# Kernel tuning notes

Measured on AMD Instinct MI355X. Metric: run time of the kernel, lower is better.

## Reference

```python
import jax, jax.numpy as jnp
import numpy as np

# Criterion init constants
WEIGHT_START = 1e-3
WEIGHT_MAX = 5e3
START_RAMPUP = 50000
N_RAMPUP = 100000
EPS = 1e-3

B, N_CLOTH, M_OBS, N_FACES = 2, 16384, 12000, 16384


def setup_inputs() -> dict:
    key = jax.random.key(0)
    ks = jax.random.split(key, 5)
    return dict(
        cloth_curr_pos=jax.random.normal(ks[0], (B, N_CLOTH, 3), jnp.float32),
        cloth_next_pos=jax.random.normal(ks[1], (B, N_CLOTH, 3), jnp.float32),
        obstacle_curr_pos=jax.random.normal(ks[2], (B, M_OBS, 3), jnp.float32),
        obstacle_next_pos=jax.random.normal(ks[3], (B, M_OBS, 3), jnp.float32),
        obstacle_faces=jax.random.randint(ks[4], (B, N_FACES, 3), 0, M_OBS, dtype=jnp.int64),
        iter_num=60000,
    )


def _face_normals(verts, faces):
    # verts: [M,3], faces: [F,3] -> normalized face normals [F,3]
    v = verts[faces]  # [F,3(vert),3(xyz)]
    n = jnp.cross(v[:, 1] - v[:, 0], v[:, 2] - v[:, 0])
    return n / (jnp.linalg.norm(n, axis=-1, keepdims=True) + 1e-12)


def _calc_loss(curr_pos, next_pos, obs_curr, obs_next, faces):
    # face centroids at current obstacle positions: [F,3]
    face_curr = obs_curr[faces].mean(axis=-2)
    # brute-force KNN (K=1): squared euclidean distances [N,F]
    d2 = (
        jnp.sum(curr_pos * curr_pos, axis=-1, keepdims=True)
        - 2.0 * curr_pos @ face_curr.T
        + jnp.sum(face_curr * face_curr, axis=-1)[None, :]
    )
    nn_idx = jnp.argmin(d2, axis=-1)  # [N]
    # face centroids / normals at next obstacle positions
    face_next = obs_next[faces].mean(axis=-2)  # [F,3]
    fn = _face_normals(obs_next, faces)        # [F,3]
    nn_points = face_next[nn_idx]   # [N,3]
    nn_normals = fn[nn_idx]         # [N,3]
    distance = jnp.sum((next_pos - nn_points) * nn_normals, axis=-1)  # [N]
    interpenetration = jnp.maximum(EPS - distance, 0.0) ** 3
    return interpenetration.sum(), interpenetration


def reference(cloth_curr_pos, cloth_next_pos, obstacle_curr_pos, obstacle_next_pos, obstacle_faces, iter_num):
    # weight ramp (Python scalar math, matches get_weight)
    it = max(iter_num - START_RAMPUP, 0)
    progress = min(it / N_RAMPUP, 1.0)
    weight = WEIGHT_START + (WEIGHT_MAX - WEIGHT_START) * progress

    losses, per_verts = jax.vmap(_calc_loss)(
        cloth_curr_pos, cloth_next_pos, obstacle_curr_pos, obstacle_next_pos, obstacle_faces
    )
    b = cloth_curr_pos.shape[0]
    loss = losses.sum() / b * weight          # scalar
    per_vert = per_verts.sum(axis=0) / b * weight  # [N]
    return loss, per_vert
```

## Files before the change

kernel.cpp:

```cpp
#include <hip/hip_runtime.h>
#include <math.h>

#define B_ 2
#define N_ 16384
#define M_ 12000
#define F_ 16384

#define P_ 128
#define TILE_ 128

typedef short bf16x8 __attribute__((ext_vector_type(8)));
typedef float f32x16 __attribute__((ext_vector_type(16)));

__device__ __host__ inline unsigned short bf16rn(float x) {
  unsigned int u = __float_as_uint(x);
  u = (u + 0x7FFFu + ((u >> 16) & 1u)) >> 16;
  return (unsigned short)u;
}
__device__ inline float bf16tof(unsigned short h) {
  return __uint_as_float(((unsigned int)h) << 16);
}

__global__ __launch_bounds__(256) void face_precomp(
    const float* __restrict__ obs_curr,
    const float* __restrict__ obs_next,
    const int* __restrict__ faces,
    float4* __restrict__ fcurr,
    float4* __restrict__ fnext,
    uint4* __restrict__ fpack,
    float* __restrict__ out) {
  int t = blockIdx.x * 256 + threadIdx.x;
  if (t == 0) out[0] = 0.0f;
  if (t >= B_ * F_) return;
  int b = t / F_;
  const float* oc = obs_curr + (size_t)b * M_ * 3;
  const float* on = obs_next + (size_t)b * M_ * 3;
  int i0 = faces[3 * (size_t)t + 0];
  int i1 = faces[3 * (size_t)t + 1];
  int i2 = faces[3 * (size_t)t + 2];

  float ax = oc[3*i0], ay = oc[3*i0+1], az = oc[3*i0+2];
  float bx = oc[3*i1], by = oc[3*i1+1], bz = oc[3*i1+2];
  float cx = oc[3*i2], cy = oc[3*i2+1], cz = oc[3*i2+2];
  float gx = (ax + bx + cx) / 3.0f;
  float gy = (ay + by + cy) / 3.0f;
  float gz = (az + bz + cz) / 3.0f;
  float w = gx*gx + gy*gy + gz*gz;
  fcurr[t] = make_float4(gx, gy, gz, w);

  float fx = -2.0f * gx, fy = -2.0f * gy, fz = -2.0f * gz;
  unsigned short fhx = bf16rn(fx), flx = bf16rn(fx - bf16tof(fhx));
  unsigned short fhy = bf16rn(fy), fly = bf16rn(fy - bf16tof(fhy));
  unsigned short fhz = bf16rn(fz), flz = bf16rn(fz - bf16tof(fhz));
  unsigned short whi = bf16rn(w),  wlo = bf16rn(w - bf16tof(whi));
  uint4 r0, r1;
  r0.x = (unsigned)fhx | ((unsigned)flx << 16);
  r0.y = r0.x;
  r0.z = (unsigned)fhy | ((unsigned)fly << 16);
  r0.w = r0.z;
  r1.x = (unsigned)fhz | ((unsigned)flz << 16);
  r1.y = r1.x;
  r1.z = (unsigned)whi | ((unsigned)wlo << 16);
  r1.w = 0;
  fpack[(size_t)t * 2 + 0] = r0;
  fpack[(size_t)t * 2 + 1] = r1;

  float nax = on[3*i0], nay = on[3*i0+1], naz = on[3*i0+2];
  float nbx = on[3*i1], nby = on[3*i1+1], nbz = on[3*i1+2];
  float ncx = on[3*i2], ncy = on[3*i2+1], ncz = on[3*i2+2];
  float hx = (nax + nbx + ncx) / 3.0f;
  float hy = (nay + nby + ncy) / 3.0f;
  float hz = (naz + nbz + ncz) / 3.0f;
  float e1x = nbx - nax, e1y = nby - nay, e1z = nbz - naz;
  float e2x = ncx - nax, e2y = ncy - nay, e2z = ncz - naz;
  float crx = e1y * e2z - e1z * e2y;
  float cry = e1z * e2x - e1x * e2z;
  float crz = e1x * e2y - e1y * e2x;
  float len = sqrtf(crx*crx + cry*cry + crz*crz);
  float inv = 1.0f / (len + 1e-12f);
  fnext[2 * (size_t)t + 0] = make_float4(hx, hy, hz, 0.0f);
  fnext[2 * (size_t)t + 1] = make_float4(crx*inv, cry*inv, crz*inv, 0.0f);
}

__global__ __launch_bounds__(256, 4) void knn_mfma32(
    const float* __restrict__ cloth_curr,
    const uint4* __restrict__ fpack,
    float* __restrict__ pmin) {
  int bid = blockIdx.x;
  int s   = bid & 7;
  int vgb = (bid >> 3) & 127;
  int b   = bid >> 10;
  int lane = threadIdx.x & 63;
  int wid  = threadIdx.x >> 6;
  int h = lane >> 5;
  int m = lane & 31;
  int vw = vgb * 128 + wid * 32;

  const float* cp = cloth_curr + ((size_t)b * N_ + vw + m) * 3;
  float cxx = cp[0], cyy = cp[1], czz = cp[2];
  unsigned short chx = bf16rn(cxx), clx = bf16rn(cxx - bf16tof(chx));
  unsigned short chy = bf16rn(cyy), cly = bf16rn(cyy - bf16tof(chy));
  unsigned short chz = bf16rn(czz), clz = bf16rn(czz - bf16tof(chz));
  const short one = (short)0x3F80;
  bf16x8 bfrag;
  if (h == 0) {
    bfrag[0] = (short)chx; bfrag[1] = (short)chx;
    bfrag[2] = (short)clx; bfrag[3] = (short)clx;
    bfrag[4] = (short)chy; bfrag[5] = (short)chy;
    bfrag[6] = (short)cly; bfrag[7] = (short)cly;
  } else {
    bfrag[0] = (short)chz; bfrag[1] = (short)chz;
    bfrag[2] = (short)clz; bfrag[3] = (short)clz;
    bfrag[4] = one; bfrag[5] = one;
    bfrag[6] = 0;   bfrag[7] = 0;
  }

  f32x16 zc;
#pragma unroll
  for (int k = 0; k < 16; ++k) zc[k] = 0.0f;

  const uint4* fp = fpack + ((size_t)b * F_ + (size_t)s * 2048 + m) * 2 + h;
  float* pout = pmin + ((size_t)(b * P_ + s * 16)) * N_ + vw + m;

  for (int part = 0; part < 16; ++part) {
    uint4 a0 = fp[0];
    uint4 a1 = fp[64];
    uint4 a2 = fp[128];
    uint4 a3 = fp[192];
    fp += 256;
    f32x16 d0 = __builtin_amdgcn_mfma_f32_32x32x16_bf16(
        __builtin_bit_cast(bf16x8, a0), bfrag, zc, 0, 0, 0);
    f32x16 d1 = __builtin_amdgcn_mfma_f32_32x32x16_bf16(
        __builtin_bit_cast(bf16x8, a1), bfrag, zc, 0, 0, 0);
    f32x16 d2 = __builtin_amdgcn_mfma_f32_32x32x16_bf16(
        __builtin_bit_cast(bf16x8, a2), bfrag, zc, 0, 0, 0);
    f32x16 d3 = __builtin_amdgcn_mfma_f32_32x32x16_bf16(
        __builtin_bit_cast(bf16x8, a3), bfrag, zc, 0, 0, 0);

    float r[8];
#pragma unroll
    for (int k = 0; k < 8; ++k) {
      float v = fminf(fminf(d0[k], d0[k + 8]), d1[k]);
      v = fminf(fminf(v, d1[k + 8]), d2[k]);
      v = fminf(fminf(v, d2[k + 8]), d3[k]);
      v = fminf(v, d3[k + 8]);
      r[k] = v;
    }
    float t1 = fminf(fminf(r[0], r[1]), r[2]);
    t1 = fminf(fminf(t1, r[3]), r[4]);
    t1 = fminf(fminf(t1, r[5]), r[6]);
    float bmin = fminf(t1, r[7]);
    bmin = fminf(bmin, __shfl_xor(bmin, 32, 64));
    if (lane < 32) *pout = bmin;
    pout += N_;
  }
}

__global__ __launch_bounds__(256) void epilogue(
    const float* __restrict__ cloth_curr,
    const float* __restrict__ cloth_next,
    const float4* __restrict__ fcurr,
    const float4* __restrict__ fnext,
    const float* __restrict__ pmin,
    const int* __restrict__ iter_num,
    float* __restrict__ out) {
  int t = blockIdx.x * 256 + threadIdx.x;
  int i = t >> 1;
  int b = t & 1;

  int it = *iter_num;
  double itc = (double)(it - 50000);
  if (itc < 0.0) itc = 0.0;
  double prog = itc / 100000.0;
  if (prog > 1.0) prog = 1.0;
  float weight = (float)(1e-3 + (5e3 - 1e-3) * prog);
  float scale = weight * 0.5f;

  float best = 3.4e38f;
  int bp = 0;
#pragma unroll 8
  for (int p = 0; p < P_; ++p) {
    float s = pmin[((size_t)(b * P_ + p)) * N_ + i];
    bool mm = s < best;
    best = mm ? s : best;
    bp = mm ? p : bp;
  }

  const float* cp = cloth_curr + ((size_t)b * N_ + i) * 3;
  float m2x = -2.0f * cp[0];
  float m2y = -2.0f * cp[1];
  float m2z = -2.0f * cp[2];
  const float4* fpp = fcurr + (size_t)b * F_ + (size_t)bp * TILE_;
  float sbest = 3.4e38f;
  int jwin = 0;
#pragma unroll 4
  for (int j = 0; j < TILE_; ++j) {
    float4 fc = fpp[j];
    float s = fmaf(m2x, fc.x, fmaf(m2y, fc.y, fmaf(m2z, fc.z, fc.w)));
    bool u = s < sbest;
    sbest = u ? s : sbest;
    jwin = u ? j : jwin;
  }
  int fidx = bp * TILE_ + jwin;

  float4 cent = fnext[2 * ((size_t)b * F_ + fidx) + 0];
  float4 nrm  = fnext[2 * ((size_t)b * F_ + fidx) + 1];
  const float* np2 = cloth_next + ((size_t)b * N_ + i) * 3;
  float dist = (np2[0] - cent.x) * nrm.x +
               (np2[1] - cent.y) * nrm.y +
               (np2[2] - cent.z) * nrm.z;
  float ip = fmaxf(1e-3f - dist, 0.0f);
  float acc = ip * ip * ip * scale;

  float pair = acc + __shfl_xor(acc, 1, 64);
  if (b == 0) out[1 + i] = pair;

  float r = acc;
#pragma unroll
  for (int off = 32; off > 0; off >>= 1) r += __shfl_down(r, off, 64);
  __shared__ float wsum[4];
  int lane = threadIdx.x & 63;
  int w = threadIdx.x >> 6;
  if (lane == 0) wsum[w] = r;
  __syncthreads();
  if (threadIdx.x == 0)
    atomicAdd(out, (wsum[0] + wsum[1]) + (wsum[2] + wsum[3]));
}

extern "C" void kernel_launch(void* const* d_in, const int* in_sizes, int n_in,
                              void* d_out, int out_size, void* d_ws, size_t ws_size,
                              hipStream_t stream) {
  const float* cloth_curr = (const float*)d_in[0];
  const float* cloth_next = (const float*)d_in[1];
  const float* obs_curr   = (const float*)d_in[2];
  const float* obs_next   = (const float*)d_in[3];
  const int*   faces      = (const int*)d_in[4];
  const int*   iter_num   = (const int*)d_in[5];
  float* out = (float*)d_out;

  char* w = (char*)d_ws;
  float4* fcurr = (float4*)(w);
  float4* fnext = (float4*)(w + 524288);
  uint4*  fpack = (uint4*)(w + 1572864);
  float*  pmin  = (float*)(w + 3670016);

  face_precomp<<<(B_ * F_ + 255) / 256, 256, 0, stream>>>(
      obs_curr, obs_next, faces, fcurr, fnext, fpack, out);

  knn_mfma32<<<2048, 256, 0, stream>>>(cloth_curr, fpack, pmin);

  epilogue<<<(2 * N_) / 256, 256, 0, stream>>>(
      cloth_curr, cloth_next, fcurr, fnext, pmin, iter_num, out);
}
```

Measured before the change: 123.2 us.

## Process two cloth-vertex groups per wave to reuse face fragments across MFMAs

Each wave now handles 64 cloth vertices, held as two B fragments, instead of 32. Every loaded face fragment feeds two MFMAs, which halves global face-pack loads per unit of work and halves the grid to 1024 blocks. Partial-min accumulation is restructured to keep running minima across the two face groups of each part. The cost is more registers per thread and fewer blocks to fill the GPU, which could lower occupancy.

```diff
diff --git a/kernel.cpp b/kernel.cpp
--- a/kernel.cpp
+++ b/kernel.cpp
@@ -88,31 +88,36 @@
     float* __restrict__ pmin) {
   int bid = blockIdx.x;
   int s   = bid & 7;
-  int vgb = (bid >> 3) & 127;
-  int b   = bid >> 10;
+  int vb  = (bid >> 3) & 63;
+  int b   = bid >> 9;
   int lane = threadIdx.x & 63;
   int wid  = threadIdx.x >> 6;
   int h = lane >> 5;
   int m = lane & 31;
-  int vw = vgb * 128 + wid * 32;
-
-  const float* cp = cloth_curr + ((size_t)b * N_ + vw + m) * 3;
-  float cxx = cp[0], cyy = cp[1], czz = cp[2];
-  unsigned short chx = bf16rn(cxx), clx = bf16rn(cxx - bf16tof(chx));
-  unsigned short chy = bf16rn(cyy), cly = bf16rn(cyy - bf16tof(chy));
-  unsigned short chz = bf16rn(czz), clz = bf16rn(czz - bf16tof(chz));
+  int vw = vb * 256 + wid * 64;
+
   const short one = (short)0x3F80;
-  bf16x8 bfrag;
-  if (h == 0) {
-    bfrag[0] = (short)chx; bfrag[1] = (short)chx;
-    bfrag[2] = (short)clx; bfrag[3] = (short)clx;
-    bfrag[4] = (short)chy; bfrag[5] = (short)chy;
-    bfrag[6] = (short)cly; bfrag[7] = (short)cly;
-  } else {
-    bfrag[0] = (short)chz; bfrag[1] = (short)chz;
-    bfrag[2] = (short)clz; bfrag[3] = (short)clz;
-    bfrag[4] = one; bfrag[5] = one;
-    bfrag[6] = 0;   bfrag[7] = 0;
+  bf16x8 bfrag0, bfrag1;
+#pragma unroll
+  for (int g = 0; g < 2; ++g) {
+    const float* cp = cloth_curr + ((size_t)b * N_ + vw + g * 32 + m) * 3;
+    float cxx = cp[0], cyy = cp[1], czz = cp[2];
+    unsigned short chx = bf16rn(cxx), clx = bf16rn(cxx - bf16tof(chx));
+    unsigned short chy = bf16rn(cyy), cly = bf16rn(cyy - bf16tof(chy));
+    unsigned short chz = bf16rn(czz), clz = bf16rn(czz - bf16tof(chz));
+    bf16x8 tq;
+    if (h == 0) {
+      tq[0] = (short)chx; tq[1] = (short)chx;
+      tq[2] = (short)clx; tq[3] = (short)clx;
+      tq[4] = (short)chy; tq[5] = (short)chy;
+      tq[6] = (short)cly; tq[7] = (short)cly;
+    } else {
+      tq[0] = (short)chz; tq[1] = (short)chz;
+      tq[2] = (short)clz; tq[3] = (short)clz;
+      tq[4] = one; tq[5] = one;
+      tq[6] = 0;   tq[7] = 0;
+    }
+    if (g == 0) bfrag0 = tq; else bfrag1 = tq;
   }
 
   f32x16 zc;
@@ -120,38 +125,46 @@
   for (int k = 0; k < 16; ++k) zc[k] = 0.0f;
 
   const uint4* fp = fpack + ((size_t)b * F_ + (size_t)s * 2048 + m) * 2 + h;
-  float* pout = pmin + ((size_t)(b * P_ + s * 16)) * N_ + vw + m;
+  float* pout = pmin + ((size_t)(b * P_ + s * 16)) * N_ + vw;
 
   for (int part = 0; part < 16; ++part) {
-    uint4 a0 = fp[0];
-    uint4 a1 = fp[64];
-    uint4 a2 = fp[128];
-    uint4 a3 = fp[192];
-    fp += 256;
-    f32x16 d0 = __builtin_amdgcn_mfma_f32_32x32x16_bf16(
-        __builtin_bit_cast(bf16x8, a0), bfrag, zc, 0, 0, 0);
-    f32x16 d1 = __builtin_amdgcn_mfma_f32_32x32x16_bf16(
-        __builtin_bit_cast(bf16x8, a1), bfrag, zc, 0, 0, 0);
-    f32x16 d2 = __builtin_amdgcn_mfma_f32_32x32x16_bf16(
-        __builtin_bit_cast(bf16x8, a2), bfrag, zc, 0, 0, 0);
-    f32x16 d3 = __builtin_amdgcn_mfma_f32_32x32x16_bf16(
-        __builtin_bit_cast(bf16x8, a3), bfrag, zc, 0, 0, 0);
-
-    float r[8];
-#pragma unroll
-    for (int k = 0; k < 8; ++k) {
-      float v = fminf(fminf(d0[k], d0[k + 8]), d1[k]);
-      v = fminf(fminf(v, d1[k + 8]), d2[k]);
-      v = fminf(fminf(v, d2[k + 8]), d3[k]);
-      v = fminf(v, d3[k + 8]);
-      r[k] = v;
+    float r0[8], r1[8];
+#pragma unroll
+    for (int k = 0; k < 8; ++k) { r0[k] = 3.4e38f; r1[k] = 3.4e38f; }
+
+#pragma unroll
+    for (int grp = 0; grp < 2; ++grp) {
+      uint4 a0 = fp[0];
+      uint4 a1 = fp[64];
+      fp += 128;
+      bf16x8 av0 = __builtin_bit_cast(bf16x8, a0);
+      bf16x8 av1 = __builtin_bit_cast(bf16x8, a1);
+      f32x16 d00 = __builtin_amdgcn_mfma_f32_32x32x16_bf16(av0, bfrag0, zc, 0, 0, 0);
+      f32x16 d01 = __builtin_amdgcn_mfma_f32_32x32x16_bf16(av0, bfrag1, zc, 0, 0, 0);
+      f32x16 d10 = __builtin_amdgcn_mfma_f32_32x32x16_bf16(av1, bfrag0, zc, 0, 0, 0);
+      f32x16 d11 = __builtin_amdgcn_mfma_f32_32x32x16_bf16(av1, bfrag1, zc, 0, 0, 0);
+#pragma unroll
+      for (int k = 0; k < 8; ++k) {
+        r0[k] = fminf(fminf(d00[k], d00[k + 8]), r0[k]);
+        r0[k] = fminf(fminf(d10[k], d10[k + 8]), r0[k]);
+        r1[k] = fminf(fminf(d01[k], d01[k + 8]), r1[k]);
+        r1[k] = fminf(fminf(d11[k], d11[k + 8]), r1[k]);
+      }
     }
-    float t1 = fminf(fminf(r[0], r[1]), r[2]);
-    t1 = fminf(fminf(t1, r[3]), r[4]);
-    t1 = fminf(fminf(t1, r[5]), r[6]);
-    float bmin = fminf(t1, r[7]);
-    bmin = fminf(bmin, __shfl_xor(bmin, 32, 64));
-    if (lane < 32) *pout = bmin;
+    float t0 = fminf(fminf(r0[0], r0[1]), r0[2]);
+    t0 = fminf(fminf(t0, r0[3]), r0[4]);
+    t0 = fminf(fminf(t0, r0[5]), r0[6]);
+    float bmin0 = fminf(t0, r0[7]);
+    float t1 = fminf(fminf(r1[0], r1[1]), r1[2]);
+    t1 = fminf(fminf(t1, r1[3]), r1[4]);
+    t1 = fminf(fminf(t1, r1[5]), r1[6]);
+    float bmin1 = fminf(t1, r1[7]);
+    bmin0 = fminf(bmin0, __shfl_xor(bmin0, 32, 64));
+    bmin1 = fminf(bmin1, __shfl_xor(bmin1, 32, 64));
+    if (lane < 32) {
+      pout[lane] = bmin0;
+      pout[32 + lane] = bmin1;
+    }
     pout += N_;
   }
 }
@@ -247,7 +260,7 @@
   face_precomp<<<(B_ * F_ + 255) / 256, 256, 0, stream>>>(
       obs_curr, obs_next, faces, fcurr, fnext, fpack, out);
 
-  knn_mfma32<<<2048, 256, 0, stream>>>(cloth_curr, fpack, pmin);
+  knn_mfma32<<<1024, 256, 0, stream>>>(cloth_curr, fpack, pmin);
 
   epilogue<<<(2 * N_) / 256, 256, 0, stream>>>(
       cloth_curr, cloth_next, fcurr, fnext, pmin, iter_num, out);
```

Result: faster. 118.5 us (-3.8%).
